# Kernel tuning notes

Hardware: AMD Instinct MI355X
Metric: run time of the kernel (lower is better)

Reference implementation:

```python
import jax, jax.numpy as jnp
import numpy as np

N_EXPERTS = 8
D_IN = 2048
D_OUT = 2048
BATCH = 8192


def setup_inputs() -> dict:
    key = jax.random.key(0)
    k_x, k_w, k_b, k_a, k_m = jax.random.split(key, 5)
    xs = jax.random.normal(k_x, (BATCH, D_IN), dtype=jnp.float32)
    # Expert parameters: each submodule modeled as Linear(D_IN, D_OUT)
    W = jax.random.normal(k_w, (N_EXPERTS, D_IN, D_OUT), dtype=jnp.float32) / np.sqrt(D_IN)
    b = jax.random.normal(k_b, (N_EXPERTS, D_OUT), dtype=jnp.float32) * 0.01
    actions = jax.random.randint(k_a, (BATCH,), 0, N_EXPERTS, dtype=jnp.int32)
    mxs = jax.random.randint(k_m, (BATCH,), 0, N_EXPERTS, dtype=jnp.int32)  # pass-through metadata
    return {"xs": xs, "W": W, "b": b, "mxs": mxs, "actions": actions}


def reference(xs, W, b, mxs, actions):
    # Original: per-sample split, route sample i to submodule actions[i], concat.
    # Vectorized MoE dispatch-combine: compute all expert outputs, select by one-hot.
    onehot = jax.nn.one_hot(actions, W.shape[0], dtype=xs.dtype)  # [B, E]
    # y_all[b,e,f] = xs[b,:] @ W[e,:,:]; combine with one-hot selection, add routed bias.
    ys = jnp.einsum('be,bd,edf->bf', onehot, xs, W) + b[actions]  # [B, D_OUT]
    return (ys, mxs, actions)
```

## Files before the change

### kernel.cpp

```cpp
#include <hip/hip_runtime.h>
#include <hip/hip_bf16.h>
#include <stdint.h>

#define BATCH 8192
#define BATCH_PAD (BATCH + 128)
#define DIN   2048
#define DOUT  2048
#define NEXP  8
#define BM    128
#define BN    128
#define BK    64

typedef __attribute__((ext_vector_type(4))) float fx4;
typedef __attribute__((ext_vector_type(8))) short sx8;

__device__ __forceinline__ short f2b(float x){
  unsigned u = __float_as_uint(x);
  u = u + 0x7FFFu + ((u >> 16) & 1u);
  return (short)(u >> 16);
}

__device__ __forceinline__ void gload16(const void* g, void* l){
  __builtin_amdgcn_global_load_lds(
      (const __attribute__((address_space(1))) unsigned int*)g,
      (__attribute__((address_space(3))) unsigned int*)l, 16, 0, 0);
}

__global__ void prep_kernel(const int* __restrict__ actions, int* __restrict__ perm,
                            int* __restrict__ cnt_off){
  __shared__ int cnt[NEXP], off[NEXP], cur[NEXP];
  int t = threadIdx.x;
  if (t < NEXP) cnt[t] = 0;
  __syncthreads();
  for (int i = t; i < BATCH; i += 256) atomicAdd(&cnt[actions[i]], 1);
  __syncthreads();
  if (t == 0){ int s = 0; for (int e = 0; e < NEXP; ++e){ off[e] = s; cur[e] = s; s += cnt[e]; } }
  __syncthreads();
  for (int i = t; i < BATCH; i += 256){
    int e = actions[i];
    int p = atomicAdd(&cur[e], 1);
    perm[p] = i;
  }
  if (t < NEXP){ cnt_off[t] = cnt[t]; cnt_off[NEXP + t] = off[t]; }
}

__global__ void gatherx_kernel(const float* __restrict__ xs, const int* __restrict__ perm,
                               short* __restrict__ xp){
  int i = blockIdx.x;
  int t = threadIdx.x;
  short v[8];
  if (i < BATCH){
    const fx4* src = (const fx4*)(xs + (size_t)perm[i] * DIN + t * 8);
    fx4 a = src[0], b2 = src[1];
    v[0]=f2b(a.x); v[1]=f2b(a.y); v[2]=f2b(a.z); v[3]=f2b(a.w);
    v[4]=f2b(b2.x); v[5]=f2b(b2.y); v[6]=f2b(b2.z); v[7]=f2b(b2.w);
  } else {
#pragma unroll
    for (int j = 0; j < 8; ++j) v[j] = 0;
  }
  *(sx8*)(xp + (size_t)i * DIN + t * 8) = *(const sx8*)v;
}

__global__ void transw_kernel(const float* __restrict__ W, short* __restrict__ Wt){
  __shared__ float tile[64][65];
  int e  = blockIdx.z;
  int n0 = blockIdx.x * 64;
  int k0 = blockIdx.y * 64;
  const float* Wp = W  + (size_t)e * DIN * DOUT;
  short*       Wo = Wt + (size_t)e * DOUT * DIN;
  int t  = threadIdx.x;
  int lr = t >> 6;
  int lc = t & 63;
#pragma unroll
  for (int j = 0; j < 16; ++j){
    int k = j * 4 + lr;
    tile[k][lc] = Wp[(size_t)(k0 + k) * DOUT + n0 + lc];
  }
  __syncthreads();
#pragma unroll
  for (int j = 0; j < 16; ++j){
    int n = j * 4 + lr;
    Wo[(size_t)(n0 + n) * DIN + k0 + lc] = f2b(tile[lc][n]);
  }
}

__global__ void tail_kernel(const int* __restrict__ mxs, const int* __restrict__ actions,
                            float* __restrict__ out){
  int i = blockIdx.x * 256 + threadIdx.x;
  if (i < BATCH){
    out[(size_t)BATCH * DOUT + i]         = (float)mxs[i];
    out[(size_t)BATCH * DOUT + BATCH + i] = (float)actions[i];
  }
}

__global__ __launch_bounds__(256)
void moe_gemm_kernel(const short* __restrict__ xp, const short* __restrict__ Wt,
                     const float* __restrict__ bias, const int* __restrict__ perm,
                     const int* __restrict__ cnt_off, float* __restrict__ out){
  int e     = blockIdx.z;
  int cnt_e = cnt_off[e];
  int slot  = blockIdx.y;
  if (slot * BM >= cnt_e) return;
  int off_e  = cnt_off[NEXP + e];
  int m_base = off_e + slot * BM;
  int m_cnt  = min(BM, cnt_e - slot * BM);
  int n0     = blockIdx.x * BN;

  __shared__ short As[BM * BK];
  __shared__ short Bs[BN * BK];

  int t    = threadIdx.x;
  int wid  = t >> 6;
  int lane = t & 63;
  int wm   = wid & 1;
  int wn   = wid >> 1;
  int lrow = lane & 15;
  int lk   = lane >> 4;

  int srow   = wid * 8 + (lane >> 3);
  int schunk = lane & 7;
  const char* ab = (const char*)xp + ((size_t)(m_base + srow) * DIN + schunk * 8) * 2;
  const char* bb = (const char*)Wt + ((size_t)e * DOUT * DIN + (size_t)(n0 + srow) * DIN + schunk * 8) * 2;

  fx4 acc[4][4];
#pragma unroll
  for (int i = 0; i < 4; ++i)
#pragma unroll
    for (int j = 0; j < 4; ++j)
      acc[i][j] = (fx4){0.f, 0.f, 0.f, 0.f};

  float bcol[4];
#pragma unroll
  for (int j = 0; j < 4; ++j)
    bcol[j] = bias[(size_t)e * DOUT + n0 + wn * 64 + j * 16 + lrow];

  const int NT = DIN / BK;

  for (int ks = 0; ks < NT; ++ks){
    size_t ko = (size_t)ks * BK * 2;
#pragma unroll
    for (int q = 0; q < 4; ++q)
      gload16(ab + (size_t)q * 32 * (DIN * 2) + ko, &As[q * 2048 + t * 8]);
#pragma unroll
    for (int q = 0; q < 4; ++q)
      gload16(bb + (size_t)q * 32 * (DIN * 2) + ko, &Bs[q * 2048 + t * 8]);

    __syncthreads();

#pragma unroll
    for (int kk = 0; kk < 2; ++kk){
      sx8 af[4], bfr[4];
#pragma unroll
      for (int i = 0; i < 4; ++i)
        af[i] = *(const sx8*)&As[(wm * 64 + i * 16 + lrow) * BK + kk * 32 + lk * 8];
#pragma unroll
      for (int j = 0; j < 4; ++j)
        bfr[j] = *(const sx8*)&Bs[(wn * 64 + j * 16 + lrow) * BK + kk * 32 + lk * 8];
#pragma unroll
      for (int i = 0; i < 4; ++i)
#pragma unroll
        for (int j = 0; j < 4; ++j)
          acc[i][j] = __builtin_amdgcn_mfma_f32_16x16x32_bf16(af[i], bfr[j], acc[i][j], 0, 0, 0);
    }

    __syncthreads();
  }

#pragma unroll
  for (int i = 0; i < 4; ++i){
    int rbase = wm * 64 + i * 16 + lk * 4;
    int prow[4];
#pragma unroll
    for (int q = 0; q < 4; ++q)
      prow[q] = (rbase + q < m_cnt) ? perm[m_base + rbase + q] : -1;
#pragma unroll
    for (int j = 0; j < 4; ++j){
      int col = n0 + wn * 64 + j * 16 + lrow;
      fx4 v = acc[i][j];
#pragma unroll
      for (int q = 0; q < 4; ++q)
        if (prow[q] >= 0)
          out[(size_t)prow[q] * DOUT + col] = v[q] + bcol[j];
    }
  }
}

extern "C" void kernel_launch(void* const* d_in, const int* in_sizes, int n_in,
                              void* d_out, int out_size, void* d_ws, size_t ws_size,
                              hipStream_t stream) {
  const float* xs      = (const float*)d_in[0];
  const float* W       = (const float*)d_in[1];
  const float* b       = (const float*)d_in[2];
  const int*   mxs     = (const int*)d_in[3];
  const int*   actions = (const int*)d_in[4];
  float* out = (float*)d_out;

  int*   perm    = (int*)d_ws;
  int*   cnt_off = perm + BATCH;
  short* Wt      = (short*)((char*)d_ws + 65536);
  short* xp      = (short*)((char*)d_ws + 65536 + (size_t)NEXP * DIN * DOUT * 2);

  hipLaunchKernelGGL(prep_kernel, dim3(1), dim3(256), 0, stream, actions, perm, cnt_off);
  hipLaunchKernelGGL(gatherx_kernel, dim3(BATCH_PAD), dim3(256), 0, stream, xs, perm, xp);
  hipLaunchKernelGGL(transw_kernel, dim3(DOUT/64, DIN/64, NEXP), dim3(256), 0, stream, W, Wt);
  hipLaunchKernelGGL(tail_kernel, dim3(BATCH/256), dim3(256), 0, stream, mxs, actions, out);
  hipLaunchKernelGGL(moe_gemm_kernel, dim3(DOUT/BN, 64, NEXP), dim3(256), 0, stream,
                     xp, Wt, b, perm, cnt_off, out);
}
```

Baseline: 188.1 us.

## Rewrite MoE GEMM with triple-buffered LDS pipeline, swizzle, larger tiles

The grouped GEMM moves to 128x256 tiles with 512 threads, a three-stage LDS ring of direct global-to-LDS loads, XOR-swizzled LDS layout, split half-step MFMA phases with explicit waitcnt and barriers, and a remapped 1D grid. The weight transpose kernel is vectorized, and the metadata tail kernel is folded into the prep kernel. The aim is to hide memory latency behind MFMA work, cut LDS bank conflicts, and remove one launch. In exchange the kernel uses 144KB of dynamic LDS and relies on hand-tuned vmcnt counts for correctness.

```diff
diff --git a/kernel.cpp b/kernel.cpp
--- a/kernel.cpp
+++ b/kernel.cpp
@@ -8,8 +8,11 @@
 #define DOUT  2048
 #define NEXP  8
 #define BM    128
-#define BN    128
+#define BN    256
 #define BK    64
+#define NT    (DIN / BK)
+#define ASZ   16384
+#define TSZ   49152
 
 typedef __attribute__((ext_vector_type(4))) float fx4;
 typedef __attribute__((ext_vector_type(8))) short sx8;
@@ -26,13 +29,18 @@
       (__attribute__((address_space(3))) unsigned int*)l, 16, 0, 0);
 }
 
-__global__ void prep_kernel(const int* __restrict__ actions, int* __restrict__ perm,
-                            int* __restrict__ cnt_off){
+__global__ void prep_kernel(const int* __restrict__ actions, const int* __restrict__ mxs,
+                            int* __restrict__ perm, int* __restrict__ cnt_off,
+                            float* __restrict__ out){
   __shared__ int cnt[NEXP], off[NEXP], cur[NEXP];
   int t = threadIdx.x;
   if (t < NEXP) cnt[t] = 0;
   __syncthreads();
-  for (int i = t; i < BATCH; i += 256) atomicAdd(&cnt[actions[i]], 1);
+  for (int i = t; i < BATCH; i += 256){
+    atomicAdd(&cnt[actions[i]], 1);
+    out[(size_t)BATCH * DOUT + i]         = (float)mxs[i];
+    out[(size_t)BATCH * DOUT + BATCH + i] = (float)actions[i];
+  }
   __syncthreads();
   if (t == 0){ int s = 0; for (int e = 0; e < NEXP; ++e){ off[e] = s; cur[e] = s; s += cnt[e]; } }
   __syncthreads();
@@ -62,127 +70,185 @@
 }
 
 __global__ void transw_kernel(const float* __restrict__ W, short* __restrict__ Wt){
-  __shared__ float tile[64][65];
+  __shared__ float tile[64][69];
   int e  = blockIdx.z;
   int n0 = blockIdx.x * 64;
   int k0 = blockIdx.y * 64;
-  const float* Wp = W  + (size_t)e * DIN * DOUT;
-  short*       Wo = Wt + (size_t)e * DOUT * DIN;
-  int t  = threadIdx.x;
-  int lr = t >> 6;
-  int lc = t & 63;
-#pragma unroll
-  for (int j = 0; j < 16; ++j){
-    int k = j * 4 + lr;
-    tile[k][lc] = Wp[(size_t)(k0 + k) * DOUT + n0 + lc];
-  }
-  __syncthreads();
-#pragma unroll
-  for (int j = 0; j < 16; ++j){
-    int n = j * 4 + lr;
-    Wo[(size_t)(n0 + n) * DIN + k0 + lc] = f2b(tile[lc][n]);
-  }
-}
-
-__global__ void tail_kernel(const int* __restrict__ mxs, const int* __restrict__ actions,
-                            float* __restrict__ out){
-  int i = blockIdx.x * 256 + threadIdx.x;
-  if (i < BATCH){
-    out[(size_t)BATCH * DOUT + i]         = (float)mxs[i];
-    out[(size_t)BATCH * DOUT + BATCH + i] = (float)actions[i];
-  }
-}
-
-__global__ __launch_bounds__(256)
+  const float* Wp = W + (size_t)e * DIN * DOUT + (size_t)k0 * DOUT + n0;
+  int t = threadIdx.x;
+#pragma unroll
+  for (int it = 0; it < 4; ++it){
+    int r = it * 16 + (t >> 4);
+    int c = (t & 15) * 4;
+    fx4 v = *(const fx4*)(Wp + (size_t)r * DOUT + c);
+    tile[r][c] = v.x; tile[r][c+1] = v.y; tile[r][c+2] = v.z; tile[r][c+3] = v.w;
+  }
+  __syncthreads();
+  int n  = t >> 2;
+  int kc = (t & 3) * 16;
+  short vv[16];
+#pragma unroll
+  for (int j = 0; j < 16; ++j) vv[j] = f2b(tile[kc + j][n]);
+  short* dst = Wt + (size_t)e * DOUT * DIN + (size_t)(n0 + n) * DIN + k0 + kc;
+  *(sx8*)dst       = *(const sx8*)vv;
+  *(sx8*)(dst + 8) = *(const sx8*)(vv + 8);
+}
+
+__global__ __launch_bounds__(512, 2)
 void moe_gemm_kernel(const short* __restrict__ xp, const short* __restrict__ Wt,
                      const float* __restrict__ bias, const int* __restrict__ perm,
                      const int* __restrict__ cnt_off, float* __restrict__ out){
-  int e     = blockIdx.z;
+  extern __shared__ char lds[];
+
+  int F    = blockIdx.x;
+  int J    = (F & 7) * 512 + (F >> 3);
+  int g    = J >> 6;
+  int slot = J & 63;
+  int e    = g >> 3;
+  int nb   = g & 7;
   int cnt_e = cnt_off[e];
-  int slot  = blockIdx.y;
   if (slot * BM >= cnt_e) return;
   int off_e  = cnt_off[NEXP + e];
   int m_base = off_e + slot * BM;
   int m_cnt  = min(BM, cnt_e - slot * BM);
-  int n0     = blockIdx.x * BN;
-
-  __shared__ short As[BM * BK];
-  __shared__ short Bs[BN * BK];
+  int n0     = nb * BN;
 
   int t    = threadIdx.x;
   int wid  = t >> 6;
-  int lane = t & 63;
+  int l    = t & 63;
   int wm   = wid & 1;
   int wn   = wid >> 1;
-  int lrow = lane & 15;
-  int lk   = lane >> 4;
-
-  int srow   = wid * 8 + (lane >> 3);
-  int schunk = lane & 7;
-  const char* ab = (const char*)xp + ((size_t)(m_base + srow) * DIN + schunk * 8) * 2;
-  const char* bb = (const char*)Wt + ((size_t)e * DOUT * DIN + (size_t)(n0 + srow) * DIN + schunk * 8) * 2;
+  int lrow = l & 15;
+  int lk   = l >> 4;
+
+  int csrc = (((t & 7) ^ ((t >> 3) & 7)) << 4);
+  const char* agp[2];
+  const char* bgp[4];
+  {
+    const char* xpB = (const char*)xp;
+    const char* wtB = (const char*)Wt + (size_t)e * ((size_t)DOUT * DIN * 2);
+#pragma unroll
+    for (int j = 0; j < 2; ++j){
+      int r = j * 64 + (t >> 3);
+      agp[j] = xpB + (size_t)(m_base + r) * (DIN * 2) + csrc;
+    }
+#pragma unroll
+    for (int j = 0; j < 4; ++j){
+      int r = j * 64 + (t >> 3);
+      bgp[j] = wtB + (size_t)(n0 + r) * (DIN * 2) + csrc;
+    }
+  }
+  int da0 = t * 16,        da1 = 8192  + t * 16;
+  int db0 = ASZ + t * 16,  db1 = ASZ + 8192 + t * 16;
+  int db2 = ASZ + 16384 + t * 16, db3 = ASZ + 24576 + t * 16;
+
+#define STG1(kt, base) do{ gload16(agp[0] + (size_t)(kt)*128, lds + (base) + da0); \
+                           gload16(agp[1] + (size_t)(kt)*128, lds + (base) + da1); \
+                           gload16(bgp[0] + (size_t)(kt)*128, lds + (base) + db0);}while(0)
+#define STG2(kt, base) do{ gload16(bgp[1] + (size_t)(kt)*128, lds + (base) + db1); \
+                           gload16(bgp[2] + (size_t)(kt)*128, lds + (base) + db2); \
+                           gload16(bgp[3] + (size_t)(kt)*128, lds + (base) + db3);}while(0)
+
+  int sw = (lrow & 7) << 4;
+  int aoff[2][4], boff[2][4];
+#pragma unroll
+  for (int kk = 0; kk < 2; ++kk){
+#pragma unroll
+    for (int m = 0; m < 4; ++m)
+      aoff[kk][m] = (wm * 64 + m * 16 + lrow) * 128 + (((kk * 4 + lk) * 16) ^ sw);
+#pragma unroll
+    for (int n = 0; n < 4; ++n)
+      boff[kk][n] = ASZ + (wn * 64 + n * 16 + lrow) * 128 + (((kk * 4 + lk) * 16) ^ sw);
+  }
 
   fx4 acc[4][4];
 #pragma unroll
-  for (int i = 0; i < 4; ++i)
-#pragma unroll
-    for (int j = 0; j < 4; ++j)
-      acc[i][j] = (fx4){0.f, 0.f, 0.f, 0.f};
+  for (int m = 0; m < 4; ++m)
+#pragma unroll
+    for (int n = 0; n < 4; ++n)
+      acc[m][n] = (fx4){0.f, 0.f, 0.f, 0.f};
 
   float bcol[4];
 #pragma unroll
-  for (int j = 0; j < 4; ++j)
-    bcol[j] = bias[(size_t)e * DOUT + n0 + wn * 64 + j * 16 + lrow];
-
-  const int NT = DIN / BK;
-
-  for (int ks = 0; ks < NT; ++ks){
-    size_t ko = (size_t)ks * BK * 2;
+  for (int n = 0; n < 4; ++n)
+    bcol[n] = bias[(size_t)e * DOUT + n0 + wn * 64 + n * 16 + lrow];
+
+  STG1(0, 0);     STG2(0, 0);
+  STG1(1, TSZ);   STG2(1, TSZ);
+  asm volatile("s_waitcnt vmcnt(6)" ::: "memory");
+  __builtin_amdgcn_s_barrier();
+  asm volatile("" ::: "memory");
+
+  sx8 a0[4], a1[4], b0[4], b1[4];
+#pragma unroll
+  for (int m = 0; m < 4; ++m) a0[m] = *(const sx8*)(lds + aoff[0][m]);
+#pragma unroll
+  for (int n = 0; n < 4; ++n) b0[n] = *(const sx8*)(lds + boff[0][n]);
+
+  int cmp = 0, nxt = TSZ, stg = 2 * TSZ;
+
+  for (int kt = 0; kt < NT; ++kt){
+#pragma unroll
+    for (int m = 0; m < 4; ++m) a1[m] = *(const sx8*)(lds + cmp + aoff[1][m]);
+#pragma unroll
+    for (int n = 0; n < 4; ++n) b1[n] = *(const sx8*)(lds + cmp + boff[1][n]);
+    if (kt + 2 < NT) STG1(kt + 2, stg);
+    __builtin_amdgcn_s_setprio(1);
+#pragma unroll
+    for (int m = 0; m < 4; ++m)
+#pragma unroll
+      for (int n = 0; n < 4; ++n)
+        acc[m][n] = __builtin_amdgcn_mfma_f32_16x16x32_bf16(a0[m], b0[n], acc[m][n], 0, 0, 0);
+    __builtin_amdgcn_s_setprio(0);
+    __builtin_amdgcn_s_barrier();
+    asm volatile("" ::: "memory");
+
+    if (kt + 2 < NT){
+      STG2(kt + 2, stg);
+      asm volatile("s_waitcnt vmcnt(6)" ::: "memory");
+    } else {
+      asm volatile("s_waitcnt vmcnt(0)" ::: "memory");
+    }
+    __builtin_amdgcn_s_barrier();
+    asm volatile("" ::: "memory");
+    if (kt + 1 < NT){
+#pragma unroll
+      for (int m = 0; m < 4; ++m) a0[m] = *(const sx8*)(lds + nxt + aoff[0][m]);
+#pragma unroll
+      for (int n = 0; n < 4; ++n) b0[n] = *(const sx8*)(lds + nxt + boff[0][n]);
+    }
+    __builtin_amdgcn_s_setprio(1);
+#pragma unroll
+    for (int m = 0; m < 4; ++m)
+#pragma unroll
+      for (int n = 0; n < 4; ++n)
+        acc[m][n] = __builtin_amdgcn_mfma_f32_16x16x32_bf16(a1[m], b1[n], acc[m][n], 0, 0, 0);
+    __builtin_amdgcn_s_setprio(0);
+    __builtin_amdgcn_s_barrier();
+    asm volatile("" ::: "memory");
+
+    int tmp = cmp; cmp = nxt; nxt = stg; stg = tmp;
+  }
+
+#pragma unroll
+  for (int m = 0; m < 4; ++m){
+    int rb = wm * 64 + m * 16 + lk * 4;
+    int prow[4];
 #pragma unroll
     for (int q = 0; q < 4; ++q)
-      gload16(ab + (size_t)q * 32 * (DIN * 2) + ko, &As[q * 2048 + t * 8]);
-#pragma unroll
-    for (int q = 0; q < 4; ++q)
-      gload16(bb + (size_t)q * 32 * (DIN * 2) + ko, &Bs[q * 2048 + t * 8]);
-
-    __syncthreads();
-
-#pragma unroll
-    for (int kk = 0; kk < 2; ++kk){
-      sx8 af[4], bfr[4];
-#pragma unroll
-      for (int i = 0; i < 4; ++i)
-        af[i] = *(const sx8*)&As[(wm * 64 + i * 16 + lrow) * BK + kk * 32 + lk * 8];
-#pragma unroll
-      for (int j = 0; j < 4; ++j)
-        bfr[j] = *(const sx8*)&Bs[(wn * 64 + j * 16 + lrow) * BK + kk * 32 + lk * 8];
-#pragma unroll
-      for (int i = 0; i < 4; ++i)
-#pragma unroll
-        for (int j = 0; j < 4; ++j)
-          acc[i][j] = __builtin_amdgcn_mfma_f32_16x16x32_bf16(af[i], bfr[j], acc[i][j], 0, 0, 0);
-    }
-
-    __syncthreads();
-  }
-
-#pragma unroll
-  for (int i = 0; i < 4; ++i){
-    int rbase = wm * 64 + i * 16 + lk * 4;
-    int prow[4];
-#pragma unroll
-    for (int q = 0; q < 4; ++q)
-      prow[q] = (rbase + q < m_cnt) ? perm[m_base + rbase + q] : -1;
-#pragma unroll
-    for (int j = 0; j < 4; ++j){
-      int col = n0 + wn * 64 + j * 16 + lrow;
-      fx4 v = acc[i][j];
+      prow[q] = (rb + q < m_cnt) ? perm[m_base + rb + q] : -1;
+#pragma unroll
+    for (int n = 0; n < 4; ++n){
+      int col = n0 + wn * 64 + n * 16 + lrow;
+      fx4 v = acc[m][n];
 #pragma unroll
       for (int q = 0; q < 4; ++q)
         if (prow[q] >= 0)
-          out[(size_t)prow[q] * DOUT + col] = v[q] + bcol[j];
-    }
-  }
+          out[(size_t)prow[q] * DOUT + col] = v[q] + bcol[n];
+    }
+  }
+#undef STG1
+#undef STG2
 }
 
 extern "C" void kernel_launch(void* const* d_in, const int* in_sizes, int n_in,
@@ -200,10 +266,9 @@
   short* Wt      = (short*)((char*)d_ws + 65536);
   short* xp      = (short*)((char*)d_ws + 65536 + (size_t)NEXP * DIN * DOUT * 2);
 
-  hipLaunchKernelGGL(prep_kernel, dim3(1), dim3(256), 0, stream, actions, perm, cnt_off);
+  hipLaunchKernelGGL(prep_kernel, dim3(1), dim3(256), 0, stream, actions, mxs, perm, cnt_off, out);
   hipLaunchKernelGGL(gatherx_kernel, dim3(BATCH_PAD), dim3(256), 0, stream, xs, perm, xp);
   hipLaunchKernelGGL(transw_kernel, dim3(DOUT/64, DIN/64, NEXP), dim3(256), 0, stream, W, Wt);
-  hipLaunchKernelGGL(tail_kernel, dim3(BATCH/256), dim3(256), 0, stream, mxs, actions, out);
-  hipLaunchKernelGGL(moe_gemm_kernel, dim3(DOUT/BN, 64, NEXP), dim3(256), 0, stream,
+  hipLaunchKernelGGL(moe_gemm_kernel, dim3(64 * 64), dim3(512), 147456, stream,
                      xp, Wt, b, perm, cnt_off, out);
 }
```

New measurement: 187.5 us. Within noise of the previous version (-0.3%).
